# Kernel tuning notes

Hardware: AMD Instinct MI355X
Metric: run time of the kernel (lower is better)

Reference implementation:

```python
import jax, jax.numpy as jnp
import numpy as np

D = 512; H = 8; DH = D // H; DFF = 4 * D; INNER = 2 * D; K = 31
B = 8; S = 1024
EPS = 1e-5


def layer_norm(x, g, b):
    m = jnp.mean(x, axis=-1, keepdims=True)
    v = jnp.mean(jnp.square(x - m), axis=-1, keepdims=True)
    return (x - m) * jax.lax.rsqrt(v + EPS) * g + b


def setup_inputs() -> dict:
    key = jax.random.key(0)
    ks = iter(jax.random.split(key, 32))
    w = lambda *s: jax.random.normal(next(ks), s, dtype=jnp.float32) * 0.02
    d = {
        "x": jax.random.normal(next(ks), (B, S, D), dtype=jnp.float32),
        # FF module 1
        "ln1_g": jnp.ones((D,)), "ln1_b": jnp.zeros((D,)),
        "ff1_w1": w(DFF, D), "ff1_b1": jnp.zeros((DFF,)),
        "ff1_w2": w(D, DFF), "ff1_b2": jnp.zeros((D,)),
        # attention
        "lna_g": jnp.ones((D,)), "lna_b": jnp.zeros((D,)),
        "qkv_w": w(3 * D, D), "qkv_b": jnp.zeros((3 * D,)),
        "out_w": w(D, D), "out_b": jnp.zeros((D,)),
        # conv module
        "lnc_g": jnp.ones((D,)), "lnc_b": jnp.zeros((D,)),
        "pw1_w": w(INNER, D), "pw1_b": jnp.zeros((INNER,)),
        "dw_w": w(D, 1, K), "dw_b": jnp.zeros((D,)),
        "bn_g": jnp.ones((D,)), "bn_b": jnp.zeros((D,)),
        "bn_mean": jnp.zeros((D,)), "bn_var": jnp.ones((D,)),
        "pw2_w": w(D, D), "pw2_b": jnp.zeros((D,)),
        # FF module 2
        "ln2_g": jnp.ones((D,)), "ln2_b": jnp.zeros((D,)),
        "ff2_w1": w(DFF, D), "ff2_b1": jnp.zeros((DFF,)),
        "ff2_w2": w(D, DFF), "ff2_b2": jnp.zeros((D,)),
        # final layer norm
        "lnf_g": jnp.ones((D,)), "lnf_b": jnp.zeros((D,)),
    }
    return d


def _ff(x, g, b, w1, b1, w2, b2):
    h = layer_norm(x, g, b)
    h = jax.nn.silu(h @ w1.T + b1)
    h = h @ w2.T + b2
    return h + x  # FeedForwardModule adds its own residual


def _attn(x, g, b, qkv_w, qkv_b, out_w, out_b):
    h = layer_norm(x, g, b)
    qkv = (h @ qkv_w.T + qkv_b).reshape(B, S, 3, H, DH)
    q, k, v = qkv[:, :, 0], qkv[:, :, 1], qkv[:, :, 2]  # [B,S,H,DH]
    scores = jnp.einsum('bqhd,bkhd->bhqk', q, k) / np.sqrt(DH).astype(np.float32)
    probs = jax.nn.softmax(scores, axis=-1)
    ctx = jnp.einsum('bhqk,bkhd->bqhd', probs, v).reshape(B, S, D)
    return ctx @ out_w.T + out_b


def _conv(x, g, b, pw1_w, pw1_b, dw_w, dw_b, bn_g, bn_b, bn_mean, bn_var, pw2_w, pw2_b):
    h = layer_norm(x, g, b)
    y = h @ pw1_w.T + pw1_b                      # [B,S,2D] pointwise conv1
    a, gate = jnp.split(y, 2, axis=-1)           # GLU along channel dim
    y = a * jax.nn.sigmoid(gate)                 # [B,S,D]
    y = y.transpose(0, 2, 1)                     # [B,D,S]
    y = jax.lax.conv_general_dilated(
        y, dw_w, window_strides=(1,), padding=((K // 2, K // 2),),
        dimension_numbers=('NCH', 'OIH', 'NCH'), feature_group_count=D)
    y = y + dw_b[None, :, None]
    y = (y - bn_mean[None, :, None]) * jax.lax.rsqrt(bn_var + EPS)[None, :, None]
    y = y * bn_g[None, :, None] + bn_b[None, :, None]
    y = jax.nn.silu(y)
    y = y.transpose(0, 2, 1)                     # [B,S,D]
    y = y @ pw2_w.T + pw2_b
    return y + x  # ConvModule adds its own residual


def reference(x, ln1_g, ln1_b, ff1_w1, ff1_b1, ff1_w2, ff1_b2,
              lna_g, lna_b, qkv_w, qkv_b, out_w, out_b,
              lnc_g, lnc_b, pw1_w, pw1_b, dw_w, dw_b,
              bn_g, bn_b, bn_mean, bn_var, pw2_w, pw2_b,
              ln2_g, ln2_b, ff2_w1, ff2_b1, ff2_w2, ff2_b2,
              lnf_g, lnf_b):
    x = x + 0.5 * _ff(x, ln1_g, ln1_b, ff1_w1, ff1_b1, ff1_w2, ff1_b2)
    x = x + _attn(x, lna_g, lna_b, qkv_w, qkv_b, out_w, out_b)
    x = x + _conv(x, lnc_g, lnc_b, pw1_w, pw1_b, dw_w, dw_b,
                  bn_g, bn_b, bn_mean, bn_var, pw2_w, pw2_b)
    x = x + 0.5 * _ff(x, ln2_g, ln2_b, ff2_w1, ff2_b1, ff2_w2, ff2_b2)
    return layer_norm(x, lnf_g, lnf_b)
```

## Files before the change

kernel.cpp:

```cpp
#include <hip/hip_runtime.h>
#include <hip/hip_bf16.h>

typedef __attribute__((ext_vector_type(8))) short bf16x8;
typedef __attribute__((ext_vector_type(4))) short bf16x4;
typedef __attribute__((ext_vector_type(4))) float f32x4;

#define NTOK 8192
#define SEQ  1024
#define NH   8

__device__ __forceinline__ float bfs2f(short s) {
  union { unsigned u; float f; } x; x.u = ((unsigned)(unsigned short)s) << 16; return x.f;
}
__device__ __forceinline__ short f2bfs(float f) {
  __hip_bfloat16 h = __float2bfloat16(f);
  return *reinterpret_cast<short*>(&h);
}
__device__ __forceinline__ float bfp2f(const __hip_bfloat16* p) {
  return bfs2f(*reinterpret_cast<const short*>(p));
}

__device__ __forceinline__ void gld16(const void* g, void* l) {
  __builtin_amdgcn_global_load_lds(
      (__attribute__((address_space(1))) void*)const_cast<void*>(g),
      (__attribute__((address_space(3))) void*)l, 16, 0, 0);
}

struct WSeg { const float* src; unsigned dst_off; unsigned nvec; };
struct WPack { WSeg s[8]; };

__global__ __launch_bounds__(256) void cast_wall_kernel(WPack p,
                                                        __hip_bfloat16* __restrict__ dst) {
  unsigned v = blockIdx.x * 256 + threadIdx.x;
#pragma unroll
  for (int t = 0; t < 8; ++t) {
    if (v < p.s[t].nvec) {
      const float* s = p.s[t].src + (size_t)v * 8;
      f32x4 a = *reinterpret_cast<const f32x4*>(s);
      f32x4 b = *reinterpret_cast<const f32x4*>(s + 4);
      bf16x8 o;
#pragma unroll
      for (int j = 0; j < 4; ++j) { o[j] = f2bfs(a[j]); o[4 + j] = f2bfs(b[j]); }
      *reinterpret_cast<bf16x8*>(reinterpret_cast<short*>(dst) +
                                 (size_t)(p.s[t].dst_off + v) * 8) = o;
      return;
    }
    v -= p.s[t].nvec;
  }
}

__global__ __launch_bounds__(256) void cast_dww_kernel(const float* __restrict__ src,
                                                       __hip_bfloat16* __restrict__ dst) {
  for (int k = 0; k < 31; ++k)
    for (int c = threadIdx.x; c < 512; c += 256)
      dst[k * 512 + c] = __float2bfloat16(src[c * 31 + k]);
}

struct PtrPack { const void* p[23]; };

__global__ __launch_bounds__(256) void cast_small_kernel(PtrPack pk,
                                                         __hip_bfloat16* __restrict__ dst) {
  constexpr int sizes[23] = {512, 512, 2048, 512, 512, 512, 1536, 512, 512, 512, 1024, 512,
                             512, 512, 512, 512, 512, 512, 512, 2048, 512, 512, 512};
  int off = 0;
  for (int t = 0; t < 23; ++t) {
    const int n = sizes[t];
    for (int i = threadIdx.x; i < n; i += 256)
      dst[off + i] = __float2bfloat16(((const float*)pk.p[t])[i]);
    off += n;
  }
}

__global__ void ws_bad_kernel(float* __restrict__ out) {
  if (threadIdx.x == 0) out[0] = 5000.f;
}

__global__ __launch_bounds__(256) void ln_kernel(const float* __restrict__ in,
                                                 const __hip_bfloat16* __restrict__ g,
                                                 const __hip_bfloat16* __restrict__ b,
                                                 __hip_bfloat16* __restrict__ out) {
  const int wv = threadIdx.x >> 6, ln = threadIdx.x & 63;
  const int row = blockIdx.x * 4 + wv;
  const float* p = in + (size_t)row * 512 + ln * 8;
  float v[8];
  {
    const f32x4* p4 = reinterpret_cast<const f32x4*>(p);
    f32x4 a = p4[0], c = p4[1];
#pragma unroll
    for (int j = 0; j < 4; ++j) { v[j] = a[j]; v[4 + j] = c[j]; }
  }
  float s = 0.f;
#pragma unroll
  for (int j = 0; j < 8; ++j) s += v[j];
  for (int m = 1; m < 64; m <<= 1) s += __shfl_xor(s, m);
  const float mean = s * (1.f / 512.f);
  float q = 0.f;
#pragma unroll
  for (int j = 0; j < 8; ++j) { float d = v[j] - mean; q += d * d; }
  for (int m = 1; m < 64; m <<= 1) q += __shfl_xor(q, m);
  const float rstd = rsqrtf(q * (1.f / 512.f) + 1e-5f);
  bf16x8 gg = *reinterpret_cast<const bf16x8*>(g + ln * 8);
  bf16x8 bb = *reinterpret_cast<const bf16x8*>(b + ln * 8);
  bf16x8 ov;
#pragma unroll
  for (int j = 0; j < 8; ++j)
    ov[j] = f2bfs((v[j] - mean) * rstd * bfs2f(gg[j]) + bfs2f(bb[j]));
  *reinterpret_cast<bf16x8*>(out + (size_t)row * 512 + ln * 8) = ov;
}

__global__ __launch_bounds__(256) void lnf_kernel(const float* __restrict__ in,
                                                  const __hip_bfloat16* __restrict__ g,
                                                  const __hip_bfloat16* __restrict__ b,
                                                  float* __restrict__ out) {
  const int wv = threadIdx.x >> 6, ln = threadIdx.x & 63;
  const int row = blockIdx.x * 4 + wv;
  const float* p = in + (size_t)row * 512 + ln * 8;
  float v[8];
  {
    const f32x4* p4 = reinterpret_cast<const f32x4*>(p);
    f32x4 a = p4[0], c = p4[1];
#pragma unroll
    for (int j = 0; j < 4; ++j) { v[j] = a[j]; v[4 + j] = c[j]; }
  }
  float s = 0.f;
#pragma unroll
  for (int j = 0; j < 8; ++j) s += v[j];
  for (int m = 1; m < 64; m <<= 1) s += __shfl_xor(s, m);
  const float mean = s * (1.f / 512.f);
  float q = 0.f;
#pragma unroll
  for (int j = 0; j < 8; ++j) { float d = v[j] - mean; q += d * d; }
  for (int m = 1; m < 64; m <<= 1) q += __shfl_xor(q, m);
  const float rstd = rsqrtf(q * (1.f / 512.f) + 1e-5f);
  bf16x8 gg = *reinterpret_cast<const bf16x8*>(g + ln * 8);
  bf16x8 bb = *reinterpret_cast<const bf16x8*>(b + ln * 8);
  f32x4 o0, o1;
#pragma unroll
  for (int j = 0; j < 4; ++j) {
    o0[j] = (v[j] - mean) * rstd * bfs2f(gg[j]) + bfs2f(bb[j]);
    o1[j] = (v[4 + j] - mean) * rstd * bfs2f(gg[4 + j]) + bfs2f(bb[4 + j]);
  }
  float* op = out + (size_t)row * 512 + ln * 8;
  *reinterpret_cast<f32x4*>(op) = o0;
  *reinterpret_cast<f32x4*>(op + 4) = o1;
}

template <int EPI>
__global__ __launch_bounds__(256, 3) void gemm_bt(const __hip_bfloat16* __restrict__ A,
                                                  const __hip_bfloat16* __restrict__ W,
                                                  const __hip_bfloat16* __restrict__ bias,
                                                  __hip_bfloat16* __restrict__ outb,
                                                  float* __restrict__ resid,
                                                  __hip_bfloat16* __restrict__ vTout,
                                                  int K, int M, float alpha, float beta) {
  __shared__ __align__(16) __hip_bfloat16 As[128 * 64];
  __shared__ __align__(16) __hip_bfloat16 Bs[128 * 64];
  const int tid = threadIdx.x;
  const int wv = tid >> 6, ln = tid & 63;
  const int hi = ln >> 4, lo = ln & 15;
  const int lo7 = lo & 7;
  const int gx = gridDim.x;
  const int nwg = gx * gridDim.y;
  const int t = blockIdx.y * gx + blockIdx.x;
  const int w = (t & 7) * (nwg >> 3) + (t >> 3);
  const int n0 = (w & (gx - 1)) * 128;
  const int m0 = (w / gx) * 128;
  const int wr = wv >> 1, wc = wv & 1;
  const int srow = ln >> 3;
  const int scolz = (((ln & 7) ^ srow) << 3);

  f32x4 acc[4][4] = {};

  for (int k0 = 0; k0 < K; k0 += 64) {
    __syncthreads();
#pragma unroll
    for (int i = 0; i < 4; ++i) {
      const int grp = i * 4 + wv;
      const int row = grp * 8 + srow;
      gld16(A + (size_t)(n0 + row) * K + k0 + scolz, As + grp * 512);
      gld16(W + (size_t)(m0 + row) * K + k0 + scolz, Bs + grp * 512);
    }
    __syncthreads();
#pragma unroll
    for (int kk2 = 0; kk2 < 2; ++kk2) {
      const int g0 = ((kk2 * 4 + hi) ^ lo7) << 3;
      bf16x8 af[4], bfr[4];
#pragma unroll
      for (int r = 0; r < 4; ++r)
        af[r] = *reinterpret_cast<const bf16x8*>(As + (wr * 64 + r * 16 + lo) * 64 + g0);
#pragma unroll
      for (int c = 0; c < 4; ++c)
        bfr[c] = *reinterpret_cast<const bf16x8*>(Bs + (wc * 64 + c * 16 + lo) * 64 + g0);
#pragma unroll
      for (int r = 0; r < 4; ++r)
#pragma unroll
        for (int c = 0; c < 4; ++c)
          acc[r][c] = __builtin_amdgcn_mfma_f32_16x16x32_bf16(af[r], bfr[c], acc[r][c], 0, 0, 0);
    }
  }

#pragma unroll
  for (int r = 0; r < 4; ++r) {
#pragma unroll
    for (int c = 0; c < 4; ++c) {
      const int m = m0 + wc * 64 + c * 16 + lo;
      const float bv = bfp2f(bias + m);
      const int nb = n0 + wr * 64 + r * 16 + hi * 4;
      if constexpr (EPI == 3) {
        if (m >= 1024) {
          const int hd = m - 1024;
          __hip_bfloat16* vp = vTout +
              ((size_t)((nb >> 10) * NH + (hd >> 6)) * 64 + (hd & 63)) * 1024 + (nb & 1023);
          bf16x4 vv;
#pragma unroll
          for (int j = 0; j < 4; ++j) vv[j] = f2bfs(acc[r][c][j] + bv);
          *reinterpret_cast<bf16x4*>(vp) = vv;
          continue;
        }
      }
#pragma unroll
      for (int j = 0; j < 4; ++j) {
        const int n = nb + j;
        float v = acc[r][c][j] + bv;
        if constexpr (EPI == 1) v = v / (1.f + __expf(-v));
        if constexpr (EPI == 2) {
          const size_t idx = (size_t)n * 512 + m;
          resid[idx] = alpha * resid[idx] + beta * v;
        } else {
          outb[(size_t)n * M + m] = __float2bfloat16(v);
        }
      }
    }
  }
}

__global__ __launch_bounds__(256, 4) void gemm64_resid(const __hip_bfloat16* __restrict__ A,
                                                       const __hip_bfloat16* __restrict__ W,
                                                       const __hip_bfloat16* __restrict__ bias,
                                                       const float* __restrict__ rsrc,
                                                       float* __restrict__ resid,
                                                       int K, float alpha, float beta) {
  __shared__ __align__(16) __hip_bfloat16 As[64 * 64];
  __shared__ __align__(16) __hip_bfloat16 Bs[128 * 64];
  const int tid = threadIdx.x;
  const int wv = tid >> 6, ln = tid & 63;
  const int hi = ln >> 4, lo = ln & 15;
  const int lo7 = lo & 7;
  const int gx = gridDim.x;
  const int nwg = gx * gridDim.y;
  const int t = blockIdx.y * gx + blockIdx.x;
  const int w = (t & 7) * (nwg >> 3) + (t >> 3);
  const int n0 = (w & (gx - 1)) * 64;
  const int m0 = (w / gx) * 128;
  const int wr = wv >> 1, wc = wv & 1;
  const int srow = ln >> 3;
  const int scolz = (((ln & 7) ^ srow) << 3);

  f32x4 acc[2][4] = {};

  for (int k0 = 0; k0 < K; k0 += 64) {
    __syncthreads();
#pragma unroll
    for (int i = 0; i < 2; ++i) {
      const int grp = i * 4 + wv;
      gld16(A + (size_t)(n0 + grp * 8 + srow) * K + k0 + scolz, As + grp * 512);
    }
#pragma unroll
    for (int i = 0; i < 4; ++i) {
      const int grp = i * 4 + wv;
      gld16(W + (size_t)(m0 + grp * 8 + srow) * K + k0 + scolz, Bs + grp * 512);
    }
    __syncthreads();
#pragma unroll
    for (int kk2 = 0; kk2 < 2; ++kk2) {
      const int g0 = ((kk2 * 4 + hi) ^ lo7) << 3;
      bf16x8 af[2], bfr[4];
#pragma unroll
      for (int r = 0; r < 2; ++r)
        af[r] = *reinterpret_cast<const bf16x8*>(As + (wr * 32 + r * 16 + lo) * 64 + g0);
#pragma unroll
      for (int c = 0; c < 4; ++c)
        bfr[c] = *reinterpret_cast<const bf16x8*>(Bs + (wc * 64 + c * 16 + lo) * 64 + g0);
#pragma unroll
      for (int r = 0; r < 2; ++r)
#pragma unroll
        for (int c = 0; c < 4; ++c)
          acc[r][c] = __builtin_amdgcn_mfma_f32_16x16x32_bf16(af[r], bfr[c], acc[r][c], 0, 0, 0);
    }
  }

#pragma unroll
  for (int r = 0; r < 2; ++r) {
#pragma unroll
    for (int c = 0; c < 4; ++c) {
      const int m = m0 + wc * 64 + c * 16 + lo;
      const float bv = bfp2f(bias + m);
#pragma unroll
      for (int j = 0; j < 4; ++j) {
        const int n = n0 + wr * 32 + r * 16 + hi * 4 + j;
        const size_t idx = (size_t)n * 512 + m;
        resid[idx] = alpha * rsrc[idx] + beta * (acc[r][c][j] + bv);
      }
    }
  }
}

__global__ __launch_bounds__(256, 2) void attn_kernel(const __hip_bfloat16* __restrict__ qkv,
                                                      const __hip_bfloat16* __restrict__ vT,
                                                      __hip_bfloat16* __restrict__ ctx) {
  __shared__ __align__(16) short Ks[2][64 * 64];
  __shared__ __align__(16) short Vs[2][64 * 64];
  __shared__ __align__(16) short P[4][16][64];
  const int tid = threadIdx.x;
  const int wv = tid >> 6, ln = tid & 63;
  const int hi = ln >> 4, lo = ln & 15;
  const int lo7 = lo & 7;
  const int blk = ((blockIdx.x & 7) << 6) | (blockIdx.x >> 3);
  const int qt = blk & 7, h = (blk >> 3) & 7, b = blk >> 6;
  const int q0 = qt * 128 + wv * 16;

  const int srow8 = ln >> 3;
  const int gsrc = (ln & 7) ^ srow8;

  bf16x8 aq0a, aq1a, aq0b, aq1b;
  {
    const __hip_bfloat16* qpa = qkv + (size_t)(b * SEQ + q0 + lo) * 1536 + h * 64 + hi * 8;
    const __hip_bfloat16* qpb = qpa + (size_t)64 * 1536;
    bf16x8 r0 = *reinterpret_cast<const bf16x8*>(qpa);
    bf16x8 r1 = *reinterpret_cast<const bf16x8*>(qpa + 32);
    bf16x8 r2 = *reinterpret_cast<const bf16x8*>(qpb);
    bf16x8 r3 = *reinterpret_cast<const bf16x8*>(qpb + 32);
#pragma unroll
    for (int j = 0; j < 8; ++j) {
      aq0a[j] = f2bfs(bfs2f(r0[j]) * 0.125f);
      aq1a[j] = f2bfs(bfs2f(r1[j]) * 0.125f);
      aq0b[j] = f2bfs(bfs2f(r2[j]) * 0.125f);
      aq1b[j] = f2bfs(bfs2f(r3[j]) * 0.125f);
    }
  }

  const __hip_bfloat16* kbase = qkv + 512 + h * 64 + (size_t)b * SEQ * 1536;
  const __hip_bfloat16* vbase = vT + (size_t)(b * NH + h) * 64 * 1024;

  f32x4 oaccA[4] = {}, oaccB[4] = {};
  float lrowA[4] = {0.f, 0.f, 0.f, 0.f};
  float lrowB[4] = {0.f, 0.f, 0.f, 0.f};

#pragma unroll
  for (int c = 0; c < 2; ++c) {
    const int r = c * 32 + wv * 8 + srow8;
    gld16(kbase + (size_t)r * 1536 + gsrc * 8, &Ks[0][(c * 32 + wv * 8) * 64]);
    gld16(vbase + (size_t)r * 1024 + gsrc * 8, &Vs[0][(c * 32 + wv * 8) * 64]);
  }
  __syncthreads();

  int cb = 0;
  for (int kt = 0; kt < 16; ++kt) {
    if (kt < 15) {
      const int kb2 = (kt + 1) * 64;
#pragma unroll
      for (int c = 0; c < 2; ++c) {
        const int r = c * 32 + wv * 8 + srow8;
        gld16(kbase + (size_t)(kb2 + r) * 1536 + gsrc * 8,
              &Ks[cb ^ 1][(c * 32 + wv * 8) * 64]);
        gld16(vbase + (size_t)r * 1024 + kb2 + gsrc * 8,
              &Vs[cb ^ 1][(c * 32 + wv * 8) * 64]);
      }
    }

    bf16x8 bk0[4], bk1[4];
#pragma unroll
    for (int nt = 0; nt < 4; ++nt) {
      const short* kr = &Ks[cb][(nt * 16 + lo) * 64];
      bk0[nt] = *reinterpret_cast<const bf16x8*>(kr + ((hi ^ lo7) << 3));
      bk1[nt] = *reinterpret_cast<const bf16x8*>(kr + (((hi + 4) ^ lo7) << 3));
    }
    f32x4 scA[4] = {}, scB[4] = {};
#pragma unroll
    for (int nt = 0; nt < 4; ++nt) {
      scA[nt] = __builtin_amdgcn_mfma_f32_16x16x32_bf16(aq0a, bk0[nt], scA[nt], 0, 0, 0);
      scA[nt] = __builtin_amdgcn_mfma_f32_16x16x32_bf16(aq1a, bk1[nt], scA[nt], 0, 0, 0);
      scB[nt] = __builtin_amdgcn_mfma_f32_16x16x32_bf16(aq0b, bk0[nt], scB[nt], 0, 0, 0);
      scB[nt] = __builtin_amdgcn_mfma_f32_16x16x32_bf16(aq1b, bk1[nt], scB[nt], 0, 0, 0);
    }

    bf16x8 bv0[4], bv1[4];
#pragma unroll
    for (int dt = 0; dt < 4; ++dt) {
      const short* vr = &Vs[cb][(dt * 16 + lo) * 64];
      bv0[dt] = *reinterpret_cast<const bf16x8*>(vr + ((hi ^ lo7) << 3));
      bv1[dt] = *reinterpret_cast<const bf16x8*>(vr + (((hi + 4) ^ lo7) << 3));
    }

#pragma unroll
    for (int j = 0; j < 4; ++j) {
      const int prow = hi * 4 + j;
      const int pswz = (prow & 7) << 3;
#pragma unroll
      for (int nt = 0; nt < 4; ++nt) {
        const float p = __expf(scA[nt][j]);
        P[wv][prow][(nt * 16 + lo) ^ pswz] = f2bfs(p);
        lrowA[j] += p;
      }
    }
    asm volatile("" ::: "memory");
    {
      const short* pr = &P[wv][lo][0];
      bf16x8 ap0 = *reinterpret_cast<const bf16x8*>(pr + ((hi ^ lo7) << 3));
      bf16x8 ap1 = *reinterpret_cast<const bf16x8*>(pr + (((hi + 4) ^ lo7) << 3));
#pragma unroll
      for (int dt = 0; dt < 4; ++dt) {
        oaccA[dt] = __builtin_amdgcn_mfma_f32_16x16x32_bf16(ap0, bv0[dt], oaccA[dt], 0, 0, 0);
        oaccA[dt] = __builtin_amdgcn_mfma_f32_16x16x32_bf16(ap1, bv1[dt], oaccA[dt], 0, 0, 0);
      }
    }
    asm volatile("" ::: "memory");

#pragma unroll
    for (int j = 0; j < 4; ++j) {
      const int prow = hi * 4 + j;
      const int pswz = (prow & 7) << 3;
#pragma unroll
      for (int nt = 0; nt < 4; ++nt) {
        const float p = __expf(scB[nt][j]);
        P[wv][prow][(nt * 16 + lo) ^ pswz] = f2bfs(p);
        lrowB[j] += p;
      }
    }
    asm volatile("" ::: "memory");
    {
      const short* pr = &P[wv][lo][0];
      bf16x8 ap0 = *reinterpret_cast<const bf16x8*>(pr + ((hi ^ lo7) << 3));
      bf16x8 ap1 = *reinterpret_cast<const bf16x8*>(pr + (((hi + 4) ^ lo7) << 3));
#pragma unroll
      for (int dt = 0; dt < 4; ++dt) {
        oaccB[dt] = __builtin_amdgcn_mfma_f32_16x16x32_bf16(ap0, bv0[dt], oaccB[dt], 0, 0, 0);
        oaccB[dt] = __builtin_amdgcn_mfma_f32_16x16x32_bf16(ap1, bv1[dt], oaccB[dt], 0, 0, 0);
      }
    }
    __syncthreads();
    cb ^= 1;
  }

#pragma unroll
  for (int j = 0; j < 4; ++j) {
    float sa = lrowA[j], sb = lrowB[j];
    sa += __shfl_xor(sa, 1); sb += __shfl_xor(sb, 1);
    sa += __shfl_xor(sa, 2); sb += __shfl_xor(sb, 2);
    sa += __shfl_xor(sa, 4); sb += __shfl_xor(sb, 4);
    sa += __shfl_xor(sa, 8); sb += __shfl_xor(sb, 8);
    lrowA[j] = sa; lrowB[j] = sb;
  }

#pragma unroll
  for (int dt = 0; dt < 4; ++dt)
#pragma unroll
    for (int j = 0; j < 4; ++j) {
      const int d = h * 64 + dt * 16 + lo;
      const int na = b * SEQ + q0 + hi * 4 + j;
      ctx[(size_t)na * 512 + d] = __float2bfloat16(oaccA[dt][j] / lrowA[j]);
      const int nb = na + 64;
      ctx[(size_t)nb * 512 + d] = __float2bfloat16(oaccB[dt][j] / lrowB[j]);
    }
}

__global__ __launch_bounds__(256) void glu8_kernel(const __hip_bfloat16* __restrict__ y,
                                                   __hip_bfloat16* __restrict__ o) {
  const int i = blockIdx.x * 256 + threadIdx.x;
  const int c8 = i & 63;
  const int n = i >> 6;
  const short* yp = reinterpret_cast<const short*>(y) + (size_t)n * 1024 + c8 * 8;
  bf16x8 a = *reinterpret_cast<const bf16x8*>(yp);
  bf16x8 g = *reinterpret_cast<const bf16x8*>(yp + 512);
  bf16x8 ov;
#pragma unroll
  for (int j = 0; j < 8; ++j) {
    const float av = bfs2f(a[j]);
    const float gv = bfs2f(g[j]);
    ov[j] = f2bfs(av / (1.f + __expf(-gv)));
  }
  *reinterpret_cast<bf16x8*>(reinterpret_cast<short*>(o) + (size_t)n * 512 + c8 * 8) = ov;
}

__global__ __launch_bounds__(256) void dwconv8_kernel(const __hip_bfloat16* __restrict__ cin,
                                                      const __hip_bfloat16* __restrict__ wkT,
                                                      const __hip_bfloat16* __restrict__ cb,
                                                      const __hip_bfloat16* __restrict__ bng,
                                                      const __hip_bfloat16* __restrict__ bnb,
                                                      const __hip_bfloat16* __restrict__ bnm,
                                                      const __hip_bfloat16* __restrict__ bnv,
                                                      __hip_bfloat16* __restrict__ outp) {
  const int i = blockIdx.x * 256 + threadIdx.x;
  const int c8 = i & 63;
  const int n = i >> 6;
  const int t = n & 1023;
  const int base = n - t;
  const int co = c8 * 8;

  float acc[8];
  {
    bf16x8 bv = *reinterpret_cast<const bf16x8*>(cb + co);
#pragma unroll
    for (int j = 0; j < 8; ++j) acc[j] = bfs2f(bv[j]);
  }
  const int k0 = (t >= 15) ? 0 : (15 - t);
  const int k1 = (t <= SEQ - 16) ? 31 : (SEQ - 1 - t + 16);
  const short* cin_s = reinterpret_cast<const short*>(cin);
  const short* wk_s = reinterpret_cast<const short*>(wkT);
  for (int k = k0; k < k1; ++k) {
    const int ts = t + k - 15;
    bf16x8 xv = *reinterpret_cast<const bf16x8*>(cin_s + (((size_t)(base + ts)) << 9) + co);
    bf16x8 wv = *reinterpret_cast<const bf16x8*>(wk_s + k * 512 + co);
#pragma unroll
    for (int j = 0; j < 8; ++j) acc[j] += bfs2f(xv[j]) * bfs2f(wv[j]);
  }
  bf16x8 g = *reinterpret_cast<const bf16x8*>(bng + co);
  bf16x8 bb = *reinterpret_cast<const bf16x8*>(bnb + co);
  bf16x8 bm = *reinterpret_cast<const bf16x8*>(bnm + co);
  bf16x8 bvv = *reinterpret_cast<const bf16x8*>(bnv + co);
  bf16x8 ov;
#pragma unroll
  for (int j = 0; j < 8; ++j) {
    const float scl = bfs2f(g[j]) * rsqrtf(bfs2f(bvv[j]) + 1e-5f);
    float v = (acc[j] - bfs2f(bm[j])) * scl + bfs2f(bb[j]);
    v = v / (1.f + __expf(-v));
    ov[j] = f2bfs(v);
  }
  *reinterpret_cast<bf16x8*>(reinterpret_cast<short*>(outp) + ((size_t)n << 9) + co) = ov;
}

extern "C" void kernel_launch(void* const* d_in, const int* in_sizes, int n_in,
                              void* d_out, int out_size, void* d_ws, size_t ws_size,
                              hipStream_t stream) {
  float* out = (float*)d_out;
  if (ws_size < ((size_t)80 << 20)) {
    ws_bad_kernel<<<1, 64, 0, stream>>>(out);
    return;
  }

  const float* x = (const float*)d_in[0];

  char* ws = (char*)d_ws;
  float*          xs = (float*)ws;
  __hip_bfloat16* t0 = (__hip_bfloat16*)(ws + ((size_t)16 << 20));
  __hip_bfloat16* t1 = (__hip_bfloat16*)(ws + ((size_t)24 << 20));
  __hip_bfloat16* t2 = (__hip_bfloat16*)(ws + ((size_t)56 << 20));
  __hip_bfloat16* wc = (__hip_bfloat16*)(ws + ((size_t)64 << 20));
  __hip_bfloat16* vT = t1 + (size_t)NTOK * 1536;

  __hip_bfloat16* wc_ff1_w1 = wc + 0;
  __hip_bfloat16* wc_ff1_w2 = wc + 1048576;
  __hip_bfloat16* wc_qkv_w  = wc + 2097152;
  __hip_bfloat16* wc_out_w  = wc + 2883584;
  __hip_bfloat16* wc_pw1_w  = wc + 3145728;
  __hip_bfloat16* wc_pw2_w  = wc + 3670016;
  __hip_bfloat16* wc_ff2_w1 = wc + 3932160;
  __hip_bfloat16* wc_ff2_w2 = wc + 4980736;
  __hip_bfloat16* wc_dwT    = wc + 6029312;
  __hip_bfloat16* sm        = wc + 6045184;
  __hip_bfloat16* c_ln1_g = sm + 0,     *c_ln1_b = sm + 512,   *c_ff1_b1 = sm + 1024;
  __hip_bfloat16* c_ff1_b2 = sm + 3072, *c_lna_g = sm + 3584,  *c_lna_b = sm + 4096;
  __hip_bfloat16* c_qkv_b = sm + 4608,  *c_out_b = sm + 6144,  *c_lnc_g = sm + 6656;
  __hip_bfloat16* c_lnc_b = sm + 7168,  *c_pw1_b = sm + 7680,  *c_dw_b = sm + 8704;
  __hip_bfloat16* c_bn_g = sm + 9216,   *c_bn_b = sm + 9728,   *c_bn_m = sm + 10240;
  __hip_bfloat16* c_bn_v = sm + 10752,  *c_pw2_b = sm + 11264, *c_ln2_g = sm + 11776;
  __hip_bfloat16* c_ln2_b = sm + 12288, *c_ff2_b1 = sm + 12800, *c_ff2_b2 = sm + 14848;
  __hip_bfloat16* c_lnf_g = sm + 15360, *c_lnf_b = sm + 15872;

  {
    WPack wp;
    wp.s[0] = {(const float*)d_in[3],  0,      131072};
    wp.s[1] = {(const float*)d_in[5],  131072, 131072};
    wp.s[2] = {(const float*)d_in[9],  262144, 98304};
    wp.s[3] = {(const float*)d_in[11], 360448, 32768};
    wp.s[4] = {(const float*)d_in[15], 393216, 65536};
    wp.s[5] = {(const float*)d_in[23], 458752, 32768};
    wp.s[6] = {(const float*)d_in[27], 491520, 131072};
    wp.s[7] = {(const float*)d_in[29], 622592, 131072};
    cast_wall_kernel<<<2944, 256, 0, stream>>>(wp, wc);
  }
  cast_dww_kernel<<<1, 256, 0, stream>>>((const float*)d_in[17], wc_dwT);
  PtrPack pk;
  const int small_idx[23] = {1, 2, 4, 6, 7, 8, 10, 12, 13, 14, 16, 18,
                             19, 20, 21, 22, 24, 25, 26, 28, 30, 31, 32};
  for (int t = 0; t < 23; ++t) pk.p[t] = d_in[small_idx[t]];
  cast_small_kernel<<<1, 256, 0, stream>>>(pk, sm);

  ln_kernel<<<2048, 256, 0, stream>>>(x, c_ln1_g, c_ln1_b, t0);
  gemm_bt<1><<<dim3(64, 16), 256, 0, stream>>>(t0, wc_ff1_w1, c_ff1_b1, t1, nullptr, nullptr, 512, 2048, 0.f, 0.f);
  gemm64_resid<<<dim3(128, 4), 256, 0, stream>>>(t1, wc_ff1_w2, c_ff1_b2, x, xs, 2048, 1.5f, 0.5f);

  ln_kernel<<<2048, 256, 0, stream>>>(xs, c_lna_g, c_lna_b, t0);
  gemm_bt<3><<<dim3(64, 12), 256, 0, stream>>>(t0, wc_qkv_w, c_qkv_b, t1, nullptr, vT, 512, 1536, 0.f, 0.f);
  attn_kernel<<<512, 256, 0, stream>>>(t1, vT, t2);
  gemm64_resid<<<dim3(128, 4), 256, 0, stream>>>(t2, wc_out_w, c_out_b, xs, xs, 512, 1.0f, 1.0f);

  ln_kernel<<<2048, 256, 0, stream>>>(xs, c_lnc_g, c_lnc_b, t0);
  gemm_bt<0><<<dim3(64, 8), 256, 0, stream>>>(t0, wc_pw1_w, c_pw1_b, t1, nullptr, nullptr, 512, 1024, 0.f, 0.f);
  glu8_kernel<<<2048, 256, 0, stream>>>(t1, t2);
  dwconv8_kernel<<<2048, 256, 0, stream>>>(t2, wc_dwT, c_dw_b, c_bn_g, c_bn_b, c_bn_m, c_bn_v, t0);
  gemm64_resid<<<dim3(128, 4), 256, 0, stream>>>(t0, wc_pw2_w, c_pw2_b, xs, xs, 512, 2.0f, 1.0f);

  ln_kernel<<<2048, 256, 0, stream>>>(xs, c_ln2_g, c_ln2_b, t0);
  gemm_bt<1><<<dim3(64, 16), 256, 0, stream>>>(t0, wc_ff2_w1, c_ff2_b1, t1, nullptr, nullptr, 512, 2048, 0.f, 0.f);
  gemm64_resid<<<dim3(128, 4), 256, 0, stream>>>(t1, wc_ff2_w2, c_ff2_b2, xs, xs, 2048, 1.5f, 0.5f);

  lnf_kernel<<<2048, 256, 0, stream>>>(xs, c_lnf_g, c_lnf_b, out);
}
```

Before: 301.9 us.

## Add 256x256-tile 8-wave pipelined GEMM with fused SiLU for FF up-projections

Adds a new 512-thread GEMM kernel that uses 256x256 output tiles, a four-buffer LDS ring loaded with global_load_lds two k-steps ahead, swizzled LDS reads and setprio around the MFMA bursts. Bias and SiLU are applied in the epilogue. It replaces the 128x128 gemm_bt<1> for both feed-forward up-projections. The aim is more operand reuse per tile and better overlap of loads with compute. In exchange the grid drops to 256 workgroups, which may underfill the GPU, and the epilogue does scalar strided bf16 stores that could be slow.

```diff
diff --git a/kernel.cpp b/kernel.cpp
--- a/kernel.cpp
+++ b/kernel.cpp
@@ -143,6 +143,127 @@
   float* op = out + (size_t)row * 512 + ln * 8;
   *reinterpret_cast<f32x4*>(op) = o0;
   *reinterpret_cast<f32x4*>(op + 4) = o1;
+}
+
+__global__ __launch_bounds__(512, 2) void gemm8p_silu(const __hip_bfloat16* __restrict__ A,
+                                                      const __hip_bfloat16* __restrict__ W,
+                                                      const __hip_bfloat16* __restrict__ bias,
+                                                      __hip_bfloat16* __restrict__ outb,
+                                                      int K, int M) {
+  __shared__ __align__(16) short LA[4][256 * 32];
+  __shared__ __align__(16) short LB[4][256 * 32];
+  const int tid = threadIdx.x;
+  const int wid = tid >> 6, ln = tid & 63;
+  const int hi = ln >> 4, lo = ln & 15;
+  const int wr = wid >> 2, wn = wid & 3;
+  const int gx = gridDim.x;
+  const int nwg = gx * gridDim.y;
+  const int t = blockIdx.y * gx + blockIdx.x;
+  const int w = (t & 7) * (nwg >> 3) + (t >> 3);
+  const int n0 = (w & (gx - 1)) * 256;
+  const int m0 = (w / gx) * 256;
+
+  const int srow = tid >> 2;
+  const int sg = (tid & 3) ^ ((tid >> 3) & 3);
+  const int rswz = (lo >> 1) & 3;
+
+  f32x4 acc[8][4] = {};
+
+  const int NKT = K >> 5;
+
+#pragma unroll
+  for (int kt = 0; kt < 2; ++kt) {
+#pragma unroll
+    for (int h = 0; h < 2; ++h)
+      gld16(A + (size_t)(n0 + h * 128 + srow) * K + kt * 32 + sg * 8,
+            &LA[kt][h * 4096 + wid * 512]);
+#pragma unroll
+    for (int h = 0; h < 2; ++h)
+      gld16(W + (size_t)(m0 + h * 128 + srow) * K + kt * 32 + sg * 8,
+            &LB[kt][h * 4096 + wid * 512]);
+  }
+
+  for (int kt = 0; kt < NKT; ++kt) {
+    const int d = kt & 3;
+    const int dn = (kt + 2) & 3;
+    if (kt < NKT - 2) {
+#pragma unroll
+      for (int h = 0; h < 2; ++h)
+        gld16(A + (size_t)(n0 + h * 128 + srow) * K + (kt + 2) * 32 + sg * 8,
+              &LA[dn][h * 4096 + wid * 512]);
+    }
+    if (kt < NKT - 2)      asm volatile("s_waitcnt vmcnt(6)" ::: "memory");
+    else if (kt == NKT - 2) asm volatile("s_waitcnt vmcnt(4)" ::: "memory");
+    else                    asm volatile("s_waitcnt vmcnt(0)" ::: "memory");
+    __builtin_amdgcn_sched_barrier(0);
+    asm volatile("" ::: "memory");
+    __builtin_amdgcn_s_barrier();
+    asm volatile("" ::: "memory");
+    __builtin_amdgcn_sched_barrier(0);
+
+    bf16x8 bfr[4];
+#pragma unroll
+    for (int nf = 0; nf < 4; ++nf) {
+      const int row = wn * 64 + nf * 16 + lo;
+      bfr[nf] = *reinterpret_cast<const bf16x8*>(&LB[d][row * 32 + ((hi ^ rswz) << 3)]);
+    }
+
+    {
+      bf16x8 af[4];
+#pragma unroll
+      for (int mf = 0; mf < 4; ++mf) {
+        const int row = wr * 128 + mf * 16 + lo;
+        af[mf] = *reinterpret_cast<const bf16x8*>(&LA[d][row * 32 + ((hi ^ rswz) << 3)]);
+      }
+      __builtin_amdgcn_s_setprio(1);
+#pragma unroll
+      for (int mf = 0; mf < 4; ++mf)
+#pragma unroll
+        for (int nf = 0; nf < 4; ++nf)
+          acc[mf][nf] = __builtin_amdgcn_mfma_f32_16x16x32_bf16(af[mf], bfr[nf], acc[mf][nf], 0, 0, 0);
+      __builtin_amdgcn_s_setprio(0);
+    }
+
+    if (kt < NKT - 2) {
+#pragma unroll
+      for (int h = 0; h < 2; ++h)
+        gld16(W + (size_t)(m0 + h * 128 + srow) * K + (kt + 2) * 32 + sg * 8,
+              &LB[dn][h * 4096 + wid * 512]);
+    }
+
+    {
+      bf16x8 af[4];
+#pragma unroll
+      for (int mf = 0; mf < 4; ++mf) {
+        const int row = wr * 128 + (mf + 4) * 16 + lo;
+        af[mf] = *reinterpret_cast<const bf16x8*>(&LA[d][row * 32 + ((hi ^ rswz) << 3)]);
+      }
+      __builtin_amdgcn_s_setprio(1);
+#pragma unroll
+      for (int mf = 0; mf < 4; ++mf)
+#pragma unroll
+        for (int nf = 0; nf < 4; ++nf)
+          acc[mf + 4][nf] = __builtin_amdgcn_mfma_f32_16x16x32_bf16(af[mf], bfr[nf], acc[mf + 4][nf], 0, 0, 0);
+      __builtin_amdgcn_s_setprio(0);
+    }
+    __builtin_amdgcn_sched_barrier(0);
+  }
+
+#pragma unroll
+  for (int mf = 0; mf < 8; ++mf) {
+#pragma unroll
+    for (int nf = 0; nf < 4; ++nf) {
+      const int m = m0 + wn * 64 + nf * 16 + lo;
+      const float bv = bfp2f(bias + m);
+#pragma unroll
+      for (int j = 0; j < 4; ++j) {
+        const int n = n0 + wr * 128 + mf * 16 + hi * 4 + j;
+        float v = acc[mf][nf][j] + bv;
+        v = v / (1.f + __expf(-v));
+        outb[(size_t)n * M + m] = __float2bfloat16(v);
+      }
+    }
+  }
 }
 
 template <int EPI>
@@ -587,7 +708,7 @@
   cast_small_kernel<<<1, 256, 0, stream>>>(pk, sm);
 
   ln_kernel<<<2048, 256, 0, stream>>>(x, c_ln1_g, c_ln1_b, t0);
-  gemm_bt<1><<<dim3(64, 16), 256, 0, stream>>>(t0, wc_ff1_w1, c_ff1_b1, t1, nullptr, nullptr, 512, 2048, 0.f, 0.f);
+  gemm8p_silu<<<dim3(32, 8), 512, 0, stream>>>(t0, wc_ff1_w1, c_ff1_b1, t1, 512, 2048);
   gemm64_resid<<<dim3(128, 4), 256, 0, stream>>>(t1, wc_ff1_w2, c_ff1_b2, x, xs, 2048, 1.5f, 0.5f);
 
   ln_kernel<<<2048, 256, 0, stream>>>(xs, c_lna_g, c_lna_b, t0);
@@ -602,7 +723,7 @@
   gemm64_resid<<<dim3(128, 4), 256, 0, stream>>>(t0, wc_pw2_w, c_pw2_b, xs, xs, 512, 2.0f, 1.0f);
 
   ln_kernel<<<2048, 256, 0, stream>>>(xs, c_ln2_g, c_ln2_b, t0);
-  gemm_bt<1><<<dim3(64, 16), 256, 0, stream>>>(t0, wc_ff2_w1, c_ff2_b1, t1, nullptr, nullptr, 512, 2048, 0.f, 0.f);
+  gemm8p_silu<<<dim3(32, 8), 512, 0, stream>>>(t0, wc_ff2_w1, c_ff2_b1, t1, 512, 2048);
   gemm64_resid<<<dim3(128, 4), 256, 0, stream>>>(t1, wc_ff2_w2, c_ff2_b2, xs, xs, 2048, 1.5f, 0.5f);
 
   lnf_kernel<<<2048, 256, 0, stream>>>(xs, c_lnf_g, c_lnf_b, out);
```

New measurement: 310.3 us. 2.8% more time.
